# Performance work log

Hardware: AMD Instinct MI355X
Metric: run time of the kernel (lower is better)

The kernel has to match this reference:

```python
import jax, jax.numpy as jnp
import numpy as np

ALPHA = 2000.0   # alpha (bandwidth penalty)
K = 8            # number of modes
MAX_N = 20       # max ADMM iterations; tol=0 -> loop always runs MAX_N-1 iters
DC = False


def setup_inputs() -> dict:
    key = jax.random.key(0)
    signal = jax.random.normal(key, (16, 8192), dtype=jnp.float32)  # (C, T)
    return {"signal": signal}


def _forward(signal):
    C, T = signal.shape
    F = 2 * T
    # mirror extension -> (C, 2T)
    f = jnp.concatenate([signal[:, :T // 2][:, ::-1], signal, signal[:, T // 2:][:, ::-1]], axis=1)
    t = jnp.linspace(1.0 / F, 1.0, F)
    freqs = (t - 0.5 - 1.0 / F).astype(jnp.float32)                  # (F,)
    # NOTE: torch.fft.fftshift with default dim shifts ALL dims (incl. channel dim);
    # jnp.fft.fftshift with axes=None matches this behavior exactly.
    f_hat = jnp.fft.fftshift(jnp.fft.fft(f))
    f_hat_plus = f_hat.at[:, :F // 2].set(0)                         # zero negative freqs
    fpos = f_hat_plus.T.astype(jnp.complex64)                        # (F, C)
    freqs_c = freqs.astype(jnp.complex64)
    fh = freqs[F // 2:]                                              # positive freqs (F/2,)
    alpha_c = jnp.complex64(ALPHA)

    omega0 = ((0.5 / K) * jnp.arange(K, dtype=jnp.float32)).astype(jnp.complex64)  # init == 1
    u0 = jnp.zeros((F, K, C), jnp.complex64)
    sum0 = jnp.zeros((F, C), jnp.complex64)

    def omega_update(u_k):                                           # u_k: (F, C)
        p = jnp.abs(u_k[F // 2:, :]) ** 2                            # (F/2, C)
        return (jnp.sum(fh @ p) / jnp.sum(p)).astype(jnp.complex64)

    def step(carry, _):
        u_prev, omega_prev, sum_uk = carry
        sum_uk = sum_uk + u_prev[:, K - 1, :] - u_prev[:, 0, :]
        us, omegas = [], []
        for k in range(K):                                           # sequential mode recurrence
            if k > 0:
                sum_uk = sum_uk + us[k - 1] - u_prev[:, k, :]
            # torch uses omega from the PREVIOUS outer iteration for all modes
            denom = 1.0 + alpha_c * jnp.square(freqs_c - omega_prev[k])   # (F,)
            u_k = (fpos - sum_uk) / denom[:, None]   # lamda_hat stays 0 (never updated in torch)
            us.append(u_k)
            if k == 0 and DC:
                omegas.append(jnp.complex64(0.0))
            else:
                omegas.append(omega_update(u_k))
        u_curr = jnp.stack(us, axis=1)                               # (F, K, C)
        omega_curr = jnp.stack(omegas)                               # (K,)
        return (u_curr, omega_curr, sum_uk), omega_curr

    (u_fin, _, _), omega_hist = jax.lax.scan(step, (u0, omega0, sum0), None, length=MAX_N - 1)
    omega = jnp.concatenate([omega0[None, :], omega_hist], axis=0)   # (MAX_N, K)

    # Hermitian completion of the half-spectrum (matches torch index assignments & order)
    pos = u_fin[F // 2:, :, :]                                       # (F/2, K, C)
    u_hat = jnp.zeros((F, K, C), jnp.complex64)
    u_hat = u_hat.at[F // 2:].set(pos)
    u_hat = u_hat.at[jnp.arange(F // 2, 0, -1)].set(jnp.conj(pos))   # overwrites bin F/2 w/ conj
    u_hat = u_hat.at[0].set(jnp.conj(u_hat[-1]))

    u_time = jnp.fft.ifft(jnp.fft.ifftshift(u_hat, axes=0), axis=0).real  # (F, K, C)
    u_c = jnp.transpose(u_time, (1, 0, 2)).astype(jnp.complex64)          # (K, F, C)
    u_c = u_c[:, F // 4:3 * F // 4, :]                                    # crop mirror -> (K, T, C)
    u_hat2 = jnp.conj(jnp.fft.fftshift(jnp.fft.fft(u_c, axis=1), axes=1)) # (K, T, C)
    u_hat2 = jnp.transpose(u_hat2, (1, 0, 2))                             # (T, K, C)
    # torch applies ifftshift with dim=-1, which is the CHANNEL dim here; replicate faithfully
    u_out = jnp.fft.ifftshift(u_c, axes=-1).real                          # (K, T, C)
    return u_out, u_hat2, omega


def reference(signal):
    return _forward(signal)
```

## Files before the change

### kernel.cpp

```cpp
#include <hip/hip_runtime.h>
#include <math.h>

#define NPAIR 131072
#define STEPS 19
#define VMD_BLOCKS 256
#define ND_BANKS 16

#define SW(a) ((a) ^ (((a) >> 5) & 31))

#define LD_RLX(p)    __hip_atomic_load((p),       __ATOMIC_RELAXED, __HIP_MEMORY_SCOPE_AGENT)
#define ST_RLX(p,v)  __hip_atomic_store((p),(v),  __ATOMIC_RELAXED, __HIP_MEMORY_SCOPE_AGENT)
#define FAA_RLX(p,v) __hip_atomic_fetch_add((p),(v),__ATOMIC_RELAXED, __HIP_MEMORY_SCOPE_AGENT)

__device__ __forceinline__ float2 cadd(float2 a, float2 b){ return make_float2(a.x+b.x, a.y+b.y); }
__device__ __forceinline__ float2 csub(float2 a, float2 b){ return make_float2(a.x-b.x, a.y-b.y); }
__device__ __forceinline__ float2 cmul(float2 a, float2 b){
    return make_float2(a.x*b.x - a.y*b.y, a.x*b.y + a.y*b.x);
}
template<int SGN>
__device__ __forceinline__ float2 imul(float2 a){
    return (SGN > 0) ? make_float2(-a.y, a.x) : make_float2(a.y, -a.x);
}

template<int SGN>
__device__ __forceinline__ void dft8(const float2* a, float2* y){
    const float C = 0.70710678118654752f;
    const float sg = (SGN > 0) ? 1.f : -1.f;
    float2 t0 = cadd(a[0], a[4]), t1 = csub(a[0], a[4]);
    float2 t2 = cadd(a[2], a[6]), t3 = imul<SGN>(csub(a[2], a[6]));
    float2 E0 = cadd(t0, t2), E2 = csub(t0, t2), E1 = cadd(t1, t3), E3 = csub(t1, t3);
    float2 s0 = cadd(a[1], a[5]), s1 = csub(a[1], a[5]);
    float2 s2 = cadd(a[3], a[7]), s3 = imul<SGN>(csub(a[3], a[7]));
    float2 O0 = cadd(s0, s2), O2 = csub(s0, s2), O1 = cadd(s1, s3), O3 = csub(s1, s3);
    float2 w1 = make_float2(C, sg * C), w3 = make_float2(-C, sg * C);
    float2 R0 = O0, R1 = cmul(O1, w1), R2 = imul<SGN>(O2), R3 = cmul(O3, w3);
    y[0] = cadd(E0, R0); y[4] = csub(E0, R0);
    y[1] = cadd(E1, R1); y[5] = csub(E1, R1);
    y[2] = cadd(E2, R2); y[6] = csub(E2, R2);
    y[3] = cadd(E3, R3); y[7] = csub(E3, R3);
}

template<int SGN>
__device__ void lds_fft8192_r8(float2* lds, int tid){
    #pragma unroll
    for (int pi = 0; pi < 4; pi++){
        int ls = 3 * pi;
        int s  = 1 << ls;
        int nn = 8192 >> ls;
        int q = tid & (s - 1);
        float2 a[8], y[8];
        #pragma unroll
        for (int r = 0; r < 8; r++) a[r] = lds[SW(tid + (r << 10))];
        __syncthreads();
        dft8<SGN>(a, y);
        int p = tid >> ls;
        float ang = (float)(2 * p) / (float)nn;
        float sn, cs;
        sincospif(SGN > 0 ? ang : -ang, &sn, &cs);
        float2 w = make_float2(cs, sn);
        float2 wk = make_float2(1.f, 0.f);
        int o = q + ((tid - q) << 3);
        lds[SW(o)] = y[0];
        #pragma unroll
        for (int k = 1; k < 8; k++){
            wk = cmul(wk, w);
            lds[SW(o + (k << ls))] = cmul(y[k], wk);
        }
        __syncthreads();
    }
    #pragma unroll
    for (int w4 = 0; w4 < 4; w4++){
        int idx = (w4 << 10) + tid;
        float2 a = lds[SW(idx)], b = lds[SW(idx + 4096)];
        lds[SW(idx)]        = cadd(a, b);
        lds[SW(idx + 4096)] = csub(a, b);
    }
    __syncthreads();
}

__global__ __launch_bounds__(1024) void k_stageA(const float* __restrict__ sig,
                                                 float2* __restrict__ FPTA,
                                                 float2* __restrict__ FPTB,
                                                 double* __restrict__ D){
    extern __shared__ float2 lds[];
    int tid  = threadIdx.x;
    int bb   = blockIdx.x;
    for (int zi = bb * 1024 + tid; zi < 5400; zi += 32768)
        D[zi] = 0.0;
    int cw   = bb >> 1, half = bb & 1;
    int cs   = (cw + 8) & 15;
    const float* sp = sig + cs * 8192;
    #pragma unroll
    for (int r = 0; r < 8; r++){
        int p = r * 1024 + tid;
        int x = 2 * p + half;
        int mx = (x < 4096) ? (4095 - x) : ((x < 12288) ? (x - 4096) : (20479 - x));
        lds[SW(p)] = make_float2(sp[mx], 0.f);
    }
    __syncthreads();
    lds_fft8192_r8<-1>(lds, tid);
    float2* dst = (half == 0 ? FPTA : FPTB) + cw * 8192;
    #pragma unroll
    for (int r = 0; r < 8; r++){
        int j = r * 1024 + tid;
        dst[j] = lds[SW(j)];
    }
}

__global__ __launch_bounds__(512, 2) void k_vmd_all(const float2* __restrict__ FPTA,
                                                    const float2* __restrict__ FPTB,
                                                    float2* __restrict__ U,
                                                    double* __restrict__ D){
    double* NDB = D;
    int*    CNT = (int*)(D + 4864);

    int tid = blockIdx.x * 512 + threadIdx.x;
    int j = tid & 8191;
    double fr = (double)j / 16384.0;
    float2 Av = FPTA[tid], Bv = FPTB[tid];
    float snw, cnw;
    sincospif(-(float)j / 8192.0f, &snw, &cnw);
    float2 tw = cmul(Bv, make_float2(cnw, snw));
    float2 fv = make_float2(Av.x + tw.x, Av.y + tw.y);
    double fx = fv.x, fy = fv.y;
    float urx[8], ury[8];
    double om[8];
    #pragma unroll
    for (int k = 0; k < 8; k++){ urx[k] = 0.f; ury[k] = 0.f; om[k] = 0.0625 * (double)k; }
    __shared__ double lred[8][16];
    __shared__ double ndls[256];
    __shared__ double om_s[8];
    int lane = threadIdx.x & 63, wv = threadIdx.x >> 6;
    int mybank = (blockIdx.x & (ND_BANKS - 1)) * 16;
    int grp = blockIdx.x >> 4;

    for (int step = 0; step < STEPS; step++){
        if (step > 0){
            #pragma unroll
            for (int k = 0; k < 8; k++) om[k] = om_s[k];
        }
        double sx = 0.0, sy = 0.0;
        #pragma unroll
        for (int k = 1; k < 8; k++){ sx += (double)urx[k]; sy += (double)ury[k]; }
        double lx = 0.0, ly = 0.0, nloc[8], dloc[8];
        #pragma unroll
        for (int k = 0; k < 8; k++){
            if (k > 0){ sx += lx - (double)urx[k]; sy += ly - (double)ury[k]; }
            double d = fr - om[k];
            double den = 1.0 + 2000.0 * d * d;
            double rden = 1.0 / den;
            double nx = (fx - sx) * rden, ny = (fy - sy) * rden;
            urx[k] = (float)nx; ury[k] = (float)ny;
            lx = nx; ly = ny;
            double pw = nx * nx + ny * ny;
            nloc[k] = fr * pw; dloc[k] = pw;
        }
        double s8[8];
        {
            bool hi = (lane & 32) != 0;
            #pragma unroll
            for (int k = 0; k < 8; k++){
                double t = hi ? nloc[k] : dloc[k];
                double r = __shfl_xor(t, 32);
                s8[k] = (hi ? dloc[k] : nloc[k]) + r;
            }
        }
        double s4v[4];
        {
            bool hi = (lane & 16) != 0;
            #pragma unroll
            for (int k = 0; k < 4; k++){
                double t = hi ? s8[k] : s8[k + 4];
                double r = __shfl_xor(t, 16);
                s4v[k] = (hi ? s8[k + 4] : s8[k]) + r;
            }
        }
        double s2v[2];
        {
            bool hi = (lane & 8) != 0;
            #pragma unroll
            for (int k = 0; k < 2; k++){
                double t = hi ? s4v[k] : s4v[k + 2];
                double r = __shfl_xor(t, 8);
                s2v[k] = (hi ? s4v[k + 2] : s4v[k]) + r;
            }
        }
        double sv;
        {
            bool hi = (lane & 4) != 0;
            double t = hi ? s2v[0] : s2v[1];
            double r = __shfl_xor(t, 4);
            sv = (hi ? s2v[1] : s2v[0]) + r;
        }
        sv += __shfl_xor(sv, 2);
        sv += __shfl_xor(sv, 1);
        if ((lane & 3) == 0) lred[wv][lane >> 2] = sv;
        __syncthreads();
        if (threadIdx.x < 16){
            double sum = 0.0;
            #pragma unroll
            for (int w = 0; w < 8; w++) sum += lred[w][threadIdx.x];
            atomicAdd(&NDB[step * 256 + mybank + threadIdx.x], sum);
        }
        __syncthreads();
        if (step < STEPS - 1){
            if (threadIdx.x == 0){
                int target = 16 * (step + 1);
                int old = FAA_RLX(&CNT[grp * 32], 1);
                bool released = false;
                if (old == target - 1){
                    int rold = FAA_RLX(&CNT[512], 1);
                    if (rold == target - 1){
                        #pragma unroll
                        for (int g = 0; g < 16; g++)
                            ST_RLX(&CNT[576 + g * 32], step + 1);
                        released = true;
                    }
                }
                if (!released)
                    while (LD_RLX(&CNT[576 + grp * 32]) <= step)
                        __builtin_amdgcn_s_sleep(1);
            }
            __syncthreads();
            if (threadIdx.x < 256)
                ndls[threadIdx.x] = LD_RLX(&NDB[step * 256 + threadIdx.x]);
            __syncthreads();
            if (threadIdx.x < 8){
                double n_ = 0.0, d_ = 0.0;
                #pragma unroll
                for (int bk = 0; bk < ND_BANKS; bk++){
                    n_ += ndls[bk * 16 + threadIdx.x];
                    d_ += ndls[bk * 16 + 8 + threadIdx.x];
                }
                om_s[threadIdx.x] = n_ / d_;
            }
            __syncthreads();
        }
    }
    #pragma unroll
    for (int k = 0; k < 8; k++) U[k * NPAIR + tid] = make_float2(urx[k], ury[k]);
}

__global__ __launch_bounds__(1024) void k_stageCD(float2* __restrict__ U){
    extern __shared__ float2 lds[];
    int tid = threadIdx.x;
    int b = blockIdx.x;
    const float2* pos = U + b * 8192;
    float* slice = (float*)(U) + (size_t)b * 16384;
    const float inv = 1.0f / 16384.0f;
    #pragma unroll
    for (int r = 0; r < 8; r++){
        int p = r * 1024 + tid;
        float2 Hk, HkM;
        if (p == 0){
            Hk  = make_float2(pos[0].x, 0.f);
            HkM = make_float2(pos[8191].x, 0.f);
        } else {
            Hk = pos[p];
            float2 q2 = pos[8192 - p];
            HkM = make_float2(q2.x, -q2.y);
        }
        float2 S  = cadd(Hk, HkM);
        float2 Dv = csub(Hk, HkM);
        float sn, cn;
        sincospif((float)p / 8192.0f, &sn, &cn);
        float2 c = cmul(make_float2(cn, sn), Dv);
        lds[SW(p)] = make_float2(S.x - c.y, S.y + c.x);
    }
    __syncthreads();
    lds_fft8192_r8<1>(lds, tid);
    float2 zreg[4];
    #pragma unroll
    for (int q = 2; q < 6; q++){
        int n = q * 1024 + tid;
        float2 z = lds[SW(n)];
        zreg[q - 2] = make_float2(z.x * inv, z.y * inv);
        *(float2*)&slice[2 * n - 4096] = zreg[q - 2];
    }
    __syncthreads();
    #pragma unroll
    for (int q = 0; q < 4; q++){
        int n = (q + 2) * 1024 + tid;
        int t = 2 * n - 4096;
        lds[SW(t)]     = make_float2(zreg[q].x, 0.f);
        lds[SW(t + 1)] = make_float2(zreg[q].y, 0.f);
    }
    __syncthreads();
    lds_fft8192_r8<-1>(lds, tid);
    #pragma unroll
    for (int q = 0; q < 8; q++){
        int t = q * 1024 + tid;
        float2 Y = lds[SW(((q + 4) & 7) * 1024 + tid)];
        slice[8192 + t] = Y.x;
    }
}

__global__ __launch_bounds__(256) void k_outs(const float* __restrict__ U32,
                                              const double* __restrict__ ndb,
                                              float* __restrict__ out){
    __shared__ float smem[128 * 65];
    int bx = blockIdx.x;
    int tid = threadIdx.x;
    if (bx < 256){
        float (*tile)[257] = (float(*)[257])smem;
        int k  = bx >> 5;
        int t0 = (bx & 31) * 256;
        #pragma unroll
        for (int cw = 0; cw < 16; cw++)
            tile[cw][tid] = U32[((size_t)(k * 16 + cw)) * 16384 + t0 + tid];
        __syncthreads();
        #pragma unroll
        for (int i = 0; i < 16; i++){
            int flat = i * 256 + tid;
            int dt = flat >> 4, ch = flat & 15;
            int cw = (ch + 8) & 15;
            out[(size_t)k * 131072 + t0 * 16 + flat] = tile[cw][dt];
        }
    } else if (bx < 384){
        float (*tile)[65] = (float(*)[65])smem;
        int t0 = (bx - 256) * 64;
        #pragma unroll
        for (int i = 0; i < 32; i++){
            int flat = i * 256 + tid;
            int b = flat >> 6, dt = flat & 63;
            tile[b][dt] = U32[(size_t)b * 16384 + 8192 + t0 + dt];
        }
        __syncthreads();
        #pragma unroll
        for (int i = 0; i < 32; i++){
            int flat = i * 256 + tid;
            int dt = flat >> 7, b = flat & 127;
            out[1048576 + (size_t)(t0 + dt) * 128 + b] = tile[b][dt];
        }
    } else {
        int t = tid;
        if (t >= 160) return;
        int row = t >> 3, k = t & 7;
        double v;
        if (row == 0){
            v = 0.0625 * (double)k;
        } else {
            const double* r = ndb + (row - 1) * 256;
            double n_ = 0.0, d_ = 0.0;
            #pragma unroll
            for (int bk = 0; bk < ND_BANKS; bk++){
                n_ += r[bk * 16 + k];
                d_ += r[bk * 16 + 8 + k];
            }
            v = n_ / d_;
        }
        out[2097152 + t] = (float)v;
    }
}

extern "C" void kernel_launch(void* const* d_in, const int* in_sizes, int n_in,
                              void* d_out, int out_size, void* d_ws, size_t ws_size,
                              hipStream_t stream){
    const float* sig = (const float*)d_in[0];
    float* out = (float*)d_out;
    char* p = (char*)d_ws;
    float2* U    = (float2*)p;
    float2* FPTA = (float2*)p;
    float2* FPTB = (float2*)(p + (size_t)1 * 1024 * 1024);
    double* D    = (double*)(p + (size_t)8 * 1024 * 1024);

    k_stageA<<<dim3(32), dim3(1024), 65536, stream>>>(sig, FPTA, FPTB, D);
    k_vmd_all<<<dim3(VMD_BLOCKS), dim3(512), 0, stream>>>(FPTA, FPTB, U, D);
    k_stageCD<<<dim3(128), dim3(1024), 65536, stream>>>(U);
    k_outs<<<dim3(385), dim3(256), 0, stream>>>((const float*)U, D, out);
}
```

Baseline: 166.2 us.

## Replace atomic omega reduction with per-block partials and use half-size real FFT

```diff
diff --git a/kernel.cpp b/kernel.cpp
--- a/kernel.cpp
+++ b/kernel.cpp
@@ -4,13 +4,17 @@
 #define NPAIR 131072
 #define STEPS 19
 #define VMD_BLOCKS 256
-#define ND_BANKS 16
 
 #define SW(a) ((a) ^ (((a) >> 5) & 31))
 
 #define LD_RLX(p)    __hip_atomic_load((p),       __ATOMIC_RELAXED, __HIP_MEMORY_SCOPE_AGENT)
 #define ST_RLX(p,v)  __hip_atomic_store((p),(v),  __ATOMIC_RELAXED, __HIP_MEMORY_SCOPE_AGENT)
 #define FAA_RLX(p,v) __hip_atomic_fetch_add((p),(v),__ATOMIC_RELAXED, __HIP_MEMORY_SCOPE_AGENT)
+
+#define D_P     0
+#define D_CNT   77824
+#define D_OHIST 78368
+#define D_TOTAL 78512
 
 __device__ __forceinline__ float2 cadd(float2 a, float2 b){ return make_float2(a.x+b.x, a.y+b.y); }
 __device__ __forceinline__ float2 csub(float2 a, float2 b){ return make_float2(a.x-b.x, a.y-b.y); }
@@ -78,6 +82,40 @@
     __syncthreads();
 }
 
+template<int SGN>
+__device__ void lds_fft4096_r8(float2* lds, int tid){
+    #pragma unroll
+    for (int pi = 0; pi < 4; pi++){
+        int ls = 3 * pi;
+        int s  = 1 << ls;
+        int nn = 4096 >> ls;
+        float2 a[8], y[8];
+        int q = tid & (s - 1);
+        if (tid < 512){
+            #pragma unroll
+            for (int r = 0; r < 8; r++) a[r] = lds[SW(tid + (r << 9))];
+        }
+        __syncthreads();
+        if (tid < 512){
+            dft8<SGN>(a, y);
+            int p = tid >> ls;
+            float ang = (float)(2 * p) / (float)nn;
+            float sn, cs;
+            sincospif(SGN > 0 ? ang : -ang, &sn, &cs);
+            float2 w = make_float2(cs, sn);
+            float2 wk = make_float2(1.f, 0.f);
+            int o = q + ((tid - q) << 3);
+            lds[SW(o)] = y[0];
+            #pragma unroll
+            for (int k = 1; k < 8; k++){
+                wk = cmul(wk, w);
+                lds[SW(o + (k << ls))] = cmul(y[k], wk);
+            }
+        }
+        __syncthreads();
+    }
+}
+
 __global__ __launch_bounds__(1024) void k_stageA(const float* __restrict__ sig,
                                                  float2* __restrict__ FPTA,
                                                  float2* __restrict__ FPTB,
@@ -85,8 +123,8 @@
     extern __shared__ float2 lds[];
     int tid  = threadIdx.x;
     int bb   = blockIdx.x;
-    for (int zi = bb * 1024 + tid; zi < 5400; zi += 32768)
-        D[zi] = 0.0;
+    int zi = bb * 1024 + tid;
+    if (zi < 544) D[D_CNT + zi] = 0.0;
     int cw   = bb >> 1, half = bb & 1;
     int cs   = (cw + 8) & 15;
     const float* sp = sig + cs * 8192;
@@ -111,8 +149,9 @@
                                                     const float2* __restrict__ FPTB,
                                                     float2* __restrict__ U,
                                                     double* __restrict__ D){
-    double* NDB = D;
-    int*    CNT = (int*)(D + 4864);
+    double* P     = D + D_P;
+    int*    CNT   = (int*)(D + D_CNT);
+    double* OHIST = D + D_OHIST;
 
     int tid = blockIdx.x * 512 + threadIdx.x;
     int j = tid & 8191;
@@ -131,7 +170,6 @@
     __shared__ double ndls[256];
     __shared__ double om_s[8];
     int lane = threadIdx.x & 63, wv = threadIdx.x >> 6;
-    int mybank = (blockIdx.x & (ND_BANKS - 1)) * 16;
     int grp = blockIdx.x >> 4;
 
     for (int step = 0; step < STEPS; step++){
@@ -200,7 +238,7 @@
             double sum = 0.0;
             #pragma unroll
             for (int w = 0; w < 8; w++) sum += lred[w][threadIdx.x];
-            atomicAdd(&NDB[step * 256 + mybank + threadIdx.x], sum);
+            ST_RLX(&P[step * 4096 + blockIdx.x * 16 + threadIdx.x], sum);
         }
         __syncthreads();
         if (step < STEPS - 1){
@@ -222,17 +260,26 @@
                         __builtin_amdgcn_s_sleep(1);
             }
             __syncthreads();
-            if (threadIdx.x < 256)
-                ndls[threadIdx.x] = LD_RLX(&NDB[step * 256 + threadIdx.x]);
+            if (threadIdx.x < 256){
+                int slot = threadIdx.x & 15, rg = threadIdx.x >> 4;
+                const double* q = &P[step * 4096 + rg * 256 + slot];
+                double s = 0.0;
+                #pragma unroll
+                for (int i = 0; i < 16; i++) s += LD_RLX(&q[i * 16]);
+                ndls[rg * 16 + slot] = s;
+            }
             __syncthreads();
             if (threadIdx.x < 8){
                 double n_ = 0.0, d_ = 0.0;
                 #pragma unroll
-                for (int bk = 0; bk < ND_BANKS; bk++){
+                for (int bk = 0; bk < 16; bk++){
                     n_ += ndls[bk * 16 + threadIdx.x];
                     d_ += ndls[bk * 16 + 8 + threadIdx.x];
                 }
-                om_s[threadIdx.x] = n_ / d_;
+                double v = n_ / d_;
+                om_s[threadIdx.x] = v;
+                if (blockIdx.x == 0)
+                    ST_RLX(&OHIST[step * 8 + threadIdx.x], v);
             }
             __syncthreads();
         }
@@ -279,26 +326,32 @@
     }
     __syncthreads();
     #pragma unroll
+    for (int q = 0; q < 4; q++)
+        lds[SW(q * 1024 + tid)] = zreg[q];
+    __syncthreads();
+    lds_fft4096_r8<-1>(lds, tid);
+    #pragma unroll
     for (int q = 0; q < 4; q++){
-        int n = (q + 2) * 1024 + tid;
-        int t = 2 * n - 4096;
-        lds[SW(t)]     = make_float2(zreg[q].x, 0.f);
-        lds[SW(t + 1)] = make_float2(zreg[q].y, 0.f);
-    }
-    __syncthreads();
-    lds_fft8192_r8<-1>(lds, tid);
-    #pragma unroll
-    for (int q = 0; q < 8; q++){
-        int t = q * 1024 + tid;
-        float2 Y = lds[SW(((q + 4) & 7) * 1024 + tid)];
-        slice[8192 + t] = Y.x;
+        int k = q * 1024 + tid;
+        float2 Wk = lds[SW(k)];
+        float2 Wm = lds[SW((4096 - k) & 4095)];
+        float ax = 0.5f * (Wk.x + Wm.x);
+        float dx = Wk.x - Wm.x, dy = Wk.y + Wm.y;
+        float bx = 0.5f * dy, by = -0.5f * dx;
+        float sn, cn;
+        sincospif(-(float)k / 4096.0f, &sn, &cn);
+        float rey = ax + cn * bx - sn * by;
+        slice[12288 + k] = rey;
+        if (k > 0) slice[12288 - k] = rey;
+        else       slice[8192]      = Wk.x - Wk.y;
     }
 }
 
 __global__ __launch_bounds__(256) void k_outs(const float* __restrict__ U32,
-                                              const double* __restrict__ ndb,
+                                              const double* __restrict__ Dbase,
                                               float* __restrict__ out){
-    __shared__ float smem[128 * 65];
+    __shared__ double smemd[128 * 65 / 2 + 140];
+    float* smem = (float*)smemd;
     int bx = blockIdx.x;
     int tid = threadIdx.x;
     if (bx < 256){
@@ -333,23 +386,36 @@
             out[1048576 + (size_t)(t0 + dt) * 128 + b] = tile[b][dt];
         }
     } else {
-        int t = tid;
-        if (t >= 160) return;
-        int row = t >> 3, k = t & 7;
-        double v;
-        if (row == 0){
-            v = 0.0625 * (double)k;
-        } else {
-            const double* r = ndb + (row - 1) * 256;
+        const double* P     = Dbase + D_P;
+        const double* OHIST = Dbase + D_OHIST;
+        double* dsm = smemd;
+        if (tid < 256){
+            int slot = tid & 15, rg = tid >> 4;
+            const double* q = &P[18 * 4096 + rg * 256 + slot];
+            double s = 0.0;
+            #pragma unroll
+            for (int i = 0; i < 16; i++) s += q[i * 16];
+            dsm[tid] = s;
+        }
+        __syncthreads();
+        if (tid < 8){
             double n_ = 0.0, d_ = 0.0;
             #pragma unroll
-            for (int bk = 0; bk < ND_BANKS; bk++){
-                n_ += r[bk * 16 + k];
-                d_ += r[bk * 16 + 8 + k];
-            }
-            v = n_ / d_;
-        }
-        out[2097152 + t] = (float)v;
+            for (int bk = 0; bk < 16; bk++){
+                n_ += dsm[bk * 16 + tid];
+                d_ += dsm[bk * 16 + 8 + tid];
+            }
+            dsm[256 + tid] = n_ / d_;
+        }
+        __syncthreads();
+        if (tid < 160){
+            int row = tid >> 3, k = tid & 7;
+            double v;
+            if (row == 0)       v = 0.0625 * (double)k;
+            else if (row <= 18) v = OHIST[(row - 1) * 8 + k];
+            else                v = dsm[256 + k];
+            out[2097152 + tid] = (float)v;
+        }
     }
 }
 
```

Result: slower. 173.4 us (+4.3%).
